# Kernel tuning notes

Hardware: AMD Instinct MI355X
Metric: run time of the kernel (lower is better)

The kernel has to match this reference:

```python
import jax, jax.numpy as jnp
import numpy as np

N_NODES = 50000   # nodes per (single) node type
N_EDGES = 1000000 # edges per edge type (avg degree ~20)
IN_SIZE = 256
OUT_SIZE = 128
N_ETYPES = 3


def setup_inputs() -> dict:
    key = jax.random.key(0)
    k0, k1, k2, k3, k4 = jax.random.split(key, 5)
    x = jax.random.normal(k0, (N_NODES, IN_SIZE), jnp.float32)
    edge_src = jax.random.randint(k1, (N_ETYPES, N_EDGES), 0, N_NODES, jnp.int32)
    edge_dst = jax.random.randint(k2, (N_ETYPES, N_EDGES), 0, N_NODES, jnp.int32)
    # per-etype Linear params (weight stored as [in, out] so Wh = x @ W + b)
    W = jax.random.normal(k3, (N_ETYPES, IN_SIZE, OUT_SIZE), jnp.float32) / np.sqrt(IN_SIZE).astype(np.float32)
    b = jax.random.normal(k4, (N_ETYPES, OUT_SIZE), jnp.float32) * 0.01
    return {"x": x, "edge_src": edge_src, "edge_dst": edge_dst, "W": W, "b": b}


def reference(x, edge_src, edge_dst, W, b):
    # Per-etype linear projection: Wh[e] = x @ W[e] + b[e]  -> [E_types, N, OUT]
    Wh = jnp.einsum('ni,eio->eno', x, W) + b[:, None, :]

    def agg_one(wh, src, dst):
        # copy_u: gather projected src features along edges  [N_EDGES, OUT]
        msgs = wh[src]
        # mean reduce onto dst nodes (scatter-mean); zero for nodes w/o in-edges
        sums = jax.ops.segment_sum(msgs, dst, num_segments=N_NODES)
        deg = jax.ops.segment_sum(jnp.ones((N_EDGES,), wh.dtype), dst, num_segments=N_NODES)
        return jnp.where(deg[:, None] > 0, sums / jnp.maximum(deg, 1.0)[:, None], 0.0)

    h = jax.vmap(agg_one)(Wh, edge_src, edge_dst)  # [E_types, N, OUT]
    # agg='stack' cross-type reducer -> [N, E_types, OUT]
    return jnp.transpose(h, (1, 0, 2))
```

## Files before the change

### kernel.cpp

```cpp
#include <hip/hip_runtime.h>

#define N_NODES 50000
#define N_EDGES 1000000
#define N_ETYPES 3
#define NB 782
#define TOTB (N_ETYPES * NB)
#define EPB 8192
#define EPT 32
#define FB  ((N_EDGES + EPB - 1) / EPB)
#define GEMMB 391
#define GCAP 2048

typedef _Float16 f16x8 __attribute__((ext_vector_type(8)));
typedef float f32x4 __attribute__((ext_vector_type(4)));

__global__ void k_prep_w(const float* __restrict__ W, _Float16* __restrict__ Wt) {
    int e  = blockIdx.y;
    int id = blockIdx.x * blockDim.x + threadIdx.x;
    int k  = id >> 7;
    int n  = id & 127;
    Wt[(size_t)e * 32768 + (size_t)n * 256 + k] =
        (_Float16)W[(size_t)e * 32768 + (size_t)k * 128 + n];
}

__global__ __launch_bounds__(256) void k_gf(
    const float* __restrict__ x,
    const _Float16* __restrict__ Wt,
    const float* __restrict__ b,
    unsigned short* __restrict__ Wh,
    const int* __restrict__ src, const int* __restrict__ dst,
    int* __restrict__ gcur, unsigned* __restrict__ grec)
{
    const int e   = blockIdx.y;
    const int tid = threadIdx.x;

    if (blockIdx.x < GEMMB) {
        const int lane = tid & 63;
        const int w    = tid >> 6;
        const int q    = lane >> 4;
        const int c    = lane & 15;
        const int rowBase = blockIdx.x * 128;
        const _Float16* Bt = Wt + (size_t)e * 32768;

        f32x4 acc[2][8];
        #pragma unroll
        for (int mt = 0; mt < 2; ++mt)
            #pragma unroll
            for (int nt = 0; nt < 8; ++nt)
                acc[mt][nt] = (f32x4){0.f, 0.f, 0.f, 0.f};

        int arow[2];
        #pragma unroll
        for (int mt = 0; mt < 2; ++mt) {
            int r = rowBase + w * 32 + mt * 16 + c;
            arow[mt] = (r < N_NODES) ? r : (N_NODES - 1);
        }

        #pragma unroll
        for (int ks = 0; ks < 8; ++ks) {
            f16x8 afrag[2];
            #pragma unroll
            for (int mt = 0; mt < 2; ++mt) {
                const float* xp = x + (size_t)arow[mt] * 256 + ks * 32 + q * 8;
                f32x4 lo = *(const f32x4*)xp;
                f32x4 hi = *(const f32x4*)(xp + 4);
                f16x8 af;
                #pragma unroll
                for (int j = 0; j < 4; ++j) {
                    af[j]     = (_Float16)lo[j];
                    af[j + 4] = (_Float16)hi[j];
                }
                afrag[mt] = af;
            }
            #pragma unroll
            for (int nt = 0; nt < 8; ++nt) {
                f16x8 bfrag = *(const f16x8*)(Bt + (size_t)(nt * 16 + c) * 256 + ks * 32 + q * 8);
                #pragma unroll
                for (int mt = 0; mt < 2; ++mt)
                    acc[mt][nt] = __builtin_amdgcn_mfma_f32_16x16x32_f16(
                        afrag[mt], bfrag, acc[mt][nt], 0, 0, 0);
            }
        }

        const size_t whBase = (size_t)e * N_NODES * 128;
        #pragma unroll
        for (int nt = 0; nt < 8; ++nt) {
            float bias = b[e * 128 + nt * 16 + c];
            #pragma unroll
            for (int mt = 0; mt < 2; ++mt) {
                int baseRow = rowBase + w * 32 + mt * 16 + q * 4;
                #pragma unroll
                for (int r = 0; r < 4; ++r) {
                    int row = baseRow + r;
                    if (row < N_NODES) {
                        float v = acc[mt][nt][r] + bias;
                        Wh[whBase + (size_t)row * 128 + nt * 16 + c] =
                            __builtin_bit_cast(unsigned short, (_Float16)v);
                    }
                }
            }
        }
    } else {
        __shared__ int lcnt[NB];
        __shared__ int lbase[NB];
        const int beg = (blockIdx.x - GEMMB) * EPB;
        const int* se = src + (size_t)e * N_EDGES;
        const int* de = dst + (size_t)e * N_EDGES;

        for (int j = tid; j < NB; j += 256) lcnt[j] = 0;
        __syncthreads();

        unsigned rec[EPT];
        int      bl [EPT];
        #pragma unroll
        for (int k = 0; k < EPT; ++k) {
            int i = beg + k * 256 + tid;
            if (i < N_EDGES) {
                int s = __builtin_nontemporal_load(se + i);
                int d = __builtin_nontemporal_load(de + i);
                int bb = d >> 6;
                int lpos = atomicAdd(&lcnt[bb], 1);
                rec[k] = (unsigned)s | ((unsigned)(d & 63) << 16);
                bl[k]  = bb | (lpos << 10);
            } else {
                bl[k] = -1;
            }
        }
        __syncthreads();
        for (int j = tid; j < NB; j += 256) {
            int c = lcnt[j];
            lbase[j] = c ? atomicAdd(&gcur[e * NB + j], c) : 0;
        }
        __syncthreads();
        #pragma unroll
        for (int k = 0; k < EPT; ++k) {
            if (bl[k] >= 0) {
                int bb   = bl[k] & 1023;
                int pos  = lbase[bb] + (bl[k] >> 10);
                if (pos < GCAP)
                    grec[(size_t)(e * NB + bb) * GCAP + pos] = rec[k];
            }
        }
    }
}

__global__ __launch_bounds__(256) void k_bagg(
    const int* __restrict__ cnt_b, const unsigned* __restrict__ grec,
    const unsigned short* __restrict__ Wh, float* __restrict__ out)
{
    __shared__ unsigned       rec_s[GCAP];
    __shared__ unsigned short nbr_s[GCAP];
    __shared__ int ndeg[64], ncur[64], nstart[64];
    const int e    = blockIdx.y;
    const int bx   = blockIdx.x;
    const int tid  = threadIdx.x;
    const int lane = tid & 63;
    const int w    = tid >> 6;
    const int half = lane >> 5;
    const int sub  = lane & 31;
    const int eb   = e * NB + bx;
    const size_t beg = (size_t)eb * GCAP;
    int m = cnt_b[eb];
    if (m > GCAP) m = GCAP;
    const unsigned* base = (const unsigned*)Wh + (size_t)e * N_NODES * 64;

    if (tid < 64) ndeg[tid] = 0;
    __syncthreads();

    for (int i = tid; i < m; i += 256) {
        unsigned r = __builtin_nontemporal_load(grec + beg + i);
        rec_s[i] = r;
        atomicAdd(&ndeg[r >> 16], 1);
    }
    __syncthreads();
    if (tid < 64) {
        int v = ndeg[tid];
        int s = v;
        #pragma unroll
        for (int d = 1; d < 64; d <<= 1) {
            int t = __shfl_up(s, d);
            if (tid >= d) s += t;
        }
        int excl = s - v;
        nstart[tid] = excl;
        ncur[tid]   = excl;
    }
    __syncthreads();
    for (int i = tid; i < m; i += 256) {
        unsigned r = rec_s[i];
        int p = atomicAdd(&ncur[r >> 16], 1);
        nbr_s[p] = (unsigned short)(r & 0xFFFFu);
    }
    __syncthreads();

    for (int t = 0; t < 16; ++t) {
        int node = w * 16 + t;
        int st = nstart[node];
        int dg = ndeg[node];
        float a0 = 0.f, a1 = 0.f, a2 = 0.f, a3 = 0.f;
        for (int c0 = 0; c0 < dg; c0 += 64) {
            int mm = dg - c0; if (mm > 64) mm = 64;
            int idx = (c0 + lane < dg) ? (int)nbr_s[st + c0 + lane] : 0;
            int fullp = mm >> 1;
            int p = 0;
            for (; p + 8 <= fullp; p += 8) {
                uint2 u[8];
                #pragma unroll
                for (int k = 0; k < 8; ++k) {
                    int r0 = 2 * (p + k);
                    int s0 = __builtin_amdgcn_readlane(idx, r0);
                    int s1 = __builtin_amdgcn_readlane(idx, r0 + 1);
                    int s  = half ? s1 : s0;
                    u[k] = *(const uint2*)(base + (size_t)s * 64 + (sub << 1));
                }
                #pragma unroll
                for (int k = 0; k < 8; ++k) {
                    a0 += (float)__builtin_bit_cast(_Float16, (unsigned short)(u[k].x & 0xFFFFu));
                    a1 += (float)__builtin_bit_cast(_Float16, (unsigned short)(u[k].x >> 16));
                    a2 += (float)__builtin_bit_cast(_Float16, (unsigned short)(u[k].y & 0xFFFFu));
                    a3 += (float)__builtin_bit_cast(_Float16, (unsigned short)(u[k].y >> 16));
                }
            }
            if (2 * p < mm) {
                uint2 u[8];
                #pragma unroll
                for (int k = 0; k < 8; ++k) {
                    int r0 = 2 * (p + k);
                    int r0c = (r0     < mm) ? r0     : 0;
                    int r1c = (r0 + 1 < mm) ? r0 + 1 : 0;
                    int s0 = __builtin_amdgcn_readlane(idx, r0c);
                    int s1 = __builtin_amdgcn_readlane(idx, r1c);
                    int s  = half ? s1 : s0;
                    u[k] = *(const uint2*)(base + (size_t)s * 64 + (sub << 1));
                }
                #pragma unroll
                for (int k = 0; k < 8; ++k) {
                    if (2 * (p + k) + half < mm) {
                        a0 += (float)__builtin_bit_cast(_Float16, (unsigned short)(u[k].x & 0xFFFFu));
                        a1 += (float)__builtin_bit_cast(_Float16, (unsigned short)(u[k].x >> 16));
                        a2 += (float)__builtin_bit_cast(_Float16, (unsigned short)(u[k].y & 0xFFFFu));
                        a3 += (float)__builtin_bit_cast(_Float16, (unsigned short)(u[k].y >> 16));
                    }
                }
            }
        }
        a0 += __shfl_xor(a0, 32);
        a1 += __shfl_xor(a1, 32);
        a2 += __shfl_xor(a2, 32);
        a3 += __shfl_xor(a3, 32);
        int n = bx * 64 + node;
        if (half == 0 && n < N_NODES) {
            float inv = (dg > 0) ? (1.0f / (float)dg) : 0.f;
            f32x4 o = {a0 * inv, a1 * inv, a2 * inv, a3 * inv};
            __builtin_nontemporal_store(o, (f32x4*)(out + (size_t)n * 384 + e * 128 + (sub << 2)));
        }
    }
}

extern "C" void kernel_launch(void* const* d_in, const int* in_sizes, int n_in,
                              void* d_out, int out_size, void* d_ws, size_t ws_size,
                              hipStream_t stream) {
    const float* x    = (const float*)d_in[0];
    const int*   esrc = (const int*)d_in[1];
    const int*   edst = (const int*)d_in[2];
    const float* W    = (const float*)d_in[3];
    const float* bias = (const float*)d_in[4];
    float*       out  = (float*)d_out;

    char* ws = (char*)d_ws;
    _Float16*       Wt  = (_Float16*)ws;
    unsigned short* Wh  = (unsigned short*)(ws + 196608);
    unsigned* grec = (unsigned*)(ws + 38596608);
    int* gcur      = (int*)(ws + 57815040);

    hipMemsetAsync(gcur, 0, TOTB * sizeof(int), stream);

    k_prep_w<<<dim3(128, 3), 256, 0, stream>>>(W, Wt);
    k_gf<<<dim3(GEMMB + FB, 3), 256, 0, stream>>>(x, Wt, bias, Wh, esrc, edst, gcur, grec);
    k_bagg<<<dim3(NB, 3), 256, 0, stream>>>(gcur, grec, Wh, out);
}
```

Measured before the change: 338.2 us.

## Remap block indices for XCD-aware scheduling and fold memset into prep kernel

Moves the 2D grids of the GEMM/fill and aggregation kernels onto flattened 1D grids with custom block-to-work mappings. GEMM blocks are grouped so that the three edge types of the same row tile run on consecutive IDs, which should keep x rows in a shared cache. Aggregation blocks are remapped so that each XCD (round-robin by blockIdx mod 8) handles a contiguous range of destination buckets, for better L2 locality. The gcur memset is folded into k_prep_w to save one launch. Padding blocks that exit early add a little overhead.

Result: faster. 324.2 us (-4.2%).

```diff
diff --git a/kernel.cpp b/kernel.cpp
--- a/kernel.cpp
+++ b/kernel.cpp
@@ -9,18 +9,23 @@
 #define EPT 32
 #define FB  ((N_EDGES + EPB - 1) / EPB)
 #define GEMMB 391
+#define GEMM_IDS 1176
+#define FILLB (FB * N_ETYPES)
 #define GCAP 2048
 
 typedef _Float16 f16x8 __attribute__((ext_vector_type(8)));
 typedef float f32x4 __attribute__((ext_vector_type(4)));
 
-__global__ void k_prep_w(const float* __restrict__ W, _Float16* __restrict__ Wt) {
+__global__ void k_prep_w(const float* __restrict__ W, _Float16* __restrict__ Wt,
+                         int* __restrict__ gcur) {
     int e  = blockIdx.y;
     int id = blockIdx.x * blockDim.x + threadIdx.x;
     int k  = id >> 7;
     int n  = id & 127;
     Wt[(size_t)e * 32768 + (size_t)n * 256 + k] =
         (_Float16)W[(size_t)e * 32768 + (size_t)k * 128 + n];
+    if (blockIdx.x == 0 && e == 0)
+        for (int j = threadIdx.x; j < TOTB; j += 256) gcur[j] = 0;
 }
 
 __global__ __launch_bounds__(256) void k_gf(
@@ -31,15 +36,20 @@
     const int* __restrict__ src, const int* __restrict__ dst,
     int* __restrict__ gcur, unsigned* __restrict__ grec)
 {
-    const int e   = blockIdx.y;
     const int tid = threadIdx.x;
 
-    if (blockIdx.x < GEMMB) {
+    if (blockIdx.x < GEMM_IDS) {
+        const int id  = blockIdx.x;
+        const int g   = id / 24;
+        const int rem = id - g * 24;
+        const int e   = rem >> 3;
+        const int bx  = g * 8 + (rem & 7);
+        if (bx >= GEMMB) return;
         const int lane = tid & 63;
         const int w    = tid >> 6;
         const int q    = lane >> 4;
         const int c    = lane & 15;
-        const int rowBase = blockIdx.x * 128;
+        const int rowBase = bx * 128;
         const _Float16* Bt = Wt + (size_t)e * 32768;
 
         f32x4 acc[2][8];
@@ -103,7 +113,10 @@
     } else {
         __shared__ int lcnt[NB];
         __shared__ int lbase[NB];
-        const int beg = (blockIdx.x - GEMMB) * EPB;
+        const int f   = blockIdx.x - GEMM_IDS;
+        const int e   = f % 3;
+        const int blk = f / 3;
+        const int beg = blk * EPB;
         const int* se = src + (size_t)e * N_EDGES;
         const int* de = dst + (size_t)e * N_EDGES;
 
@@ -151,8 +164,13 @@
     __shared__ unsigned       rec_s[GCAP];
     __shared__ unsigned short nbr_s[GCAP];
     __shared__ int ndeg[64], ncur[64], nstart[64];
-    const int e    = blockIdx.y;
-    const int bx   = blockIdx.x;
+    const int r = blockIdx.x & 7;
+    const int qq = blockIdx.x >> 3;
+    const int cnt_r = (r < 2) ? 294 : 293;
+    if (qq >= cnt_r) return;
+    const int v  = r * 293 + ((r < 2) ? r : 2) + qq;
+    const int e  = v / NB;
+    const int bx = v - e * NB;
     const int tid  = threadIdx.x;
     const int lane = tid & 63;
     const int w    = tid >> 6;
@@ -168,28 +186,28 @@
     __syncthreads();
 
     for (int i = tid; i < m; i += 256) {
-        unsigned r = __builtin_nontemporal_load(grec + beg + i);
-        rec_s[i] = r;
-        atomicAdd(&ndeg[r >> 16], 1);
+        unsigned rr_ = __builtin_nontemporal_load(grec + beg + i);
+        rec_s[i] = rr_;
+        atomicAdd(&ndeg[rr_ >> 16], 1);
     }
     __syncthreads();
     if (tid < 64) {
-        int v = ndeg[tid];
-        int s = v;
+        int vv = ndeg[tid];
+        int s = vv;
         #pragma unroll
         for (int d = 1; d < 64; d <<= 1) {
             int t = __shfl_up(s, d);
             if (tid >= d) s += t;
         }
-        int excl = s - v;
+        int excl = s - vv;
         nstart[tid] = excl;
         ncur[tid]   = excl;
     }
     __syncthreads();
     for (int i = tid; i < m; i += 256) {
-        unsigned r = rec_s[i];
-        int p = atomicAdd(&ncur[r >> 16], 1);
-        nbr_s[p] = (unsigned short)(r & 0xFFFFu);
+        unsigned rr_ = rec_s[i];
+        int p = atomicAdd(&ncur[rr_ >> 16], 1);
+        nbr_s[p] = (unsigned short)(rr_ & 0xFFFFu);
     }
     __syncthreads();
 
@@ -273,9 +291,7 @@
     unsigned* grec = (unsigned*)(ws + 38596608);
     int* gcur      = (int*)(ws + 57815040);
 
-    hipMemsetAsync(gcur, 0, TOTB * sizeof(int), stream);
-
-    k_prep_w<<<dim3(128, 3), 256, 0, stream>>>(W, Wt);
-    k_gf<<<dim3(GEMMB + FB, 3), 256, 0, stream>>>(x, Wt, bias, Wh, esrc, edst, gcur, grec);
-    k_bagg<<<dim3(NB, 3), 256, 0, stream>>>(gcur, grec, Wh, out);
-}
+    k_prep_w<<<dim3(128, 3), 256, 0, stream>>>(W, Wt, gcur);
+    k_gf<<<GEMM_IDS + FILLB, 256, 0, stream>>>(x, Wt, bias, Wh, esrc, edst, gcur, grec);
+    k_bagg<<<2352, 256, 0, stream>>>(gcur, grec, Wh, out);
+}
```
